# Kernel optimization log

Measured on AMD Instinct MI355X. Metric: run time of the kernel, lower is better.

Reference implementation:

```python
import jax, jax.numpy as jnp
import numpy as np

H = 128  # hidden size
I = 5    # input size


def setup_inputs() -> dict:
    key = jax.random.key(0)
    ks = jax.random.split(key, 8)
    B, T = 2048, 512
    s_ih = 1.0 / np.sqrt(H)
    x = jax.random.normal(ks[0], (B, T, I), dtype=jnp.float32)
    # PyTorch LSTM params, gate order (i, f, g, o)
    W_ih = jax.random.uniform(ks[1], (4 * H, I), jnp.float32, -s_ih, s_ih)
    W_hh = jax.random.uniform(ks[2], (4 * H, H), jnp.float32, -s_ih, s_ih)
    b_ih = jax.random.uniform(ks[3], (4 * H,), jnp.float32, -s_ih, s_ih)
    b_hh = jax.random.uniform(ks[4], (4 * H,), jnp.float32, -s_ih, s_ih)
    W_lin = jax.random.uniform(ks[5], (1, H), jnp.float32, -s_ih, s_ih)
    b_lin = jax.random.uniform(ks[6], (1,), jnp.float32, -s_ih, s_ih)
    return {"x": x, "W_ih": W_ih, "W_hh": W_hh, "b_ih": b_ih,
            "b_hh": b_hh, "W_lin": W_lin, "b_lin": b_lin}


def _lstm_final_h(x, W_ih, W_hh, b_ih, b_hh):
    B = x.shape[0]
    # Precompute input projection for all timesteps: [B, T, 4H]
    x_proj = jnp.einsum('bti,gi->btg', x, W_ih) + b_ih + b_hh

    def step(carry, xt):
        h, c = carry
        gates = xt + h @ W_hh.T  # [B, 4H]
        i, f, g, o = jnp.split(gates, 4, axis=-1)
        i = jax.nn.sigmoid(i)
        f = jax.nn.sigmoid(f)
        g = jnp.tanh(g)
        o = jax.nn.sigmoid(o)
        c = f * c + i * g
        h = o * jnp.tanh(c)
        return (h, c), None

    h0 = jnp.zeros((B, H), dtype=x.dtype)
    c0 = jnp.zeros((B, H), dtype=x.dtype)
    (h_n, _), _ = jax.lax.scan(step, (h0, c0), jnp.swapaxes(x_proj, 0, 1))
    return h_n  # [B, H]


def reference(x, W_ih, W_hh, b_ih, b_hh, W_lin, b_lin):
    h_n = _lstm_final_h(x, W_ih, W_hh, b_ih, b_hh)
    # h_n.reshape(num_layers*B, H) @ linear -> [B, 1]
    return h_n @ W_lin.T + b_lin
```

## Files before the change

### kernel.cpp

```cpp
#include <hip/hip_runtime.h>


#define HH 128
#define II 5
#define TT 512
#define BT 8
#define NT 512
#define KS 136
#define XT (TT * 8 + 8)
#define HB (16 * KS)

typedef __attribute__((ext_vector_type(8))) _Float16 half8;
typedef __attribute__((ext_vector_type(4))) _Float16 half4;
typedef __attribute__((ext_vector_type(4))) float f32x4;

#define SIG(u) __builtin_amdgcn_rcpf(1.0f + __builtin_amdgcn_exp2f(u))
#define MF32(A, B, C) __builtin_amdgcn_mfma_f32_16x16x32_f16((A), (B), (C), 0, 0, 0)
#define MF16(A, B, C) __builtin_amdgcn_mfma_f32_16x16x16f16((A), (B), (C), 0, 0, 0)
#define SGB(m, n) __builtin_amdgcn_sched_group_barrier((m), (n), 0)

#define STEP(PB, LAST) {                                                        \
    const _Float16* hp = hrd + (PB) * HB;                                       \
    ah0 = *reinterpret_cast<const half8*>(hp);                                  \
    ah1 = *reinterpret_cast<const half8*>(hp + 32);                             \
    ah2 = *reinterpret_cast<const half8*>(hp + 64);                             \
    ah3 = *reinterpret_cast<const half8*>(hp + 96);                             \
                    \
    f32x4 a0 = MF16(ax4, wfx[0], zero4);                                        \
    f32x4 a1 = MF16(ax4, wfx[1], zero4);                                        \
    f32x4 a2 = MF16(ax4, wfx[2], zero4);                                        \
    f32x4 a3 = MF16(ax4, wfx[3], zero4);                                        \
                                                     \
    a0 = MF32(ah0, wf[0][0], a0); a1 = MF32(ah0, wf[1][0], a1);                 \
    a0 = MF32(ah1, wf[0][1], a0); a1 = MF32(ah1, wf[1][1], a1);                 \
    a0 = MF32(ah2, wf[0][2], a0); a1 = MF32(ah2, wf[1][2], a1);                 \
    a0 = MF32(ah3, wf[0][3], a0); a1 = MF32(ah3, wf[1][3], a1);                 \
                  \
    float iv0 = SIG(a0[0]);                                                     \
    float iv1 = SIG(a0[1]);                                                     \
    float fv0 = SIG(a1[0]);                                                     \
    float fv1 = SIG(a1[1]);                                                     \
                                                     \
    a2 = MF32(ah0, wf[2][0], a2); a3 = MF32(ah0, wf[3][0], a3);                 \
    a2 = MF32(ah1, wf[2][1], a2); a3 = MF32(ah1, wf[3][1], a3);                 \
    a2 = MF32(ah2, wf[2][2], a2); a3 = MF32(ah2, wf[3][2], a3);                 \
    a2 = MF32(ah3, wf[2][3], a2); a3 = MF32(ah3, wf[3][3], a3);                 \
    if (!(LAST)) {                             \
        xcur += xinc;                                                           \
        ax4 = *reinterpret_cast<const half4*>(xcur);                            \
    }                                                                           \
    float gv0 = 1.0f - 2.0f * SIG(a2[0]);                                       \
    float ov0 = SIG(a3[0]);                                                     \
    cc0 = fv0 * cc0 + iv0 * gv0;                                                \
    float hv0 = ov0 * (1.0f - 2.0f * SIG(2.88539008f * cc0));                   \
    float gv1 = 1.0f - 2.0f * SIG(a2[1]);                                       \
    float ov1 = SIG(a3[1]);                                                     \
    cc1 = fv1 * cc1 + iv1 * gv1;                                                \
    float hv1 = ov1 * (1.0f - 2.0f * SIG(2.88539008f * cc1));                   \
    if (LAST) {                                                                 \
        hsc[bcell][hcol] = hv0; hsc[bcell + 1][hcol] = hv1;                     \
    } else {                                                                    \
        _Float16* wp = hwr + ((PB) ^ 1) * HB;                                   \
        wp[0]  = (_Float16)hv0;                                                 \
        wp[KS] = (_Float16)hv1;                                                 \
    }                                                                           \
     \
    SGB(0x100, 4);                                    \
    SGB(0x008, 4);               \
    SGB(0x008, 8);                                         \
    SGB(0x402, 14);                     \
    SGB(0x008, 8);                                         \
    __syncthreads();                                                            \
}

__global__ __launch_bounds__(NT)
__attribute__((amdgpu_waves_per_eu(2, 2)))
void lstm_r15(const float* __restrict__ x,
              const float* __restrict__ W_ih,
              const float* __restrict__ W_hh,
              const float* __restrict__ b_ih,
              const float* __restrict__ b_hh,
              const float* __restrict__ W_lin,
              const float* __restrict__ b_lin,
              float* __restrict__ out,
              int B)
{
    __shared__ __align__(16) _Float16 hbuf[2][16][KS];
    __shared__ __align__(16) _Float16 zrow[KS];
    __shared__ __align__(16) _Float16 xs[BT * XT];
    __shared__ float hsc[BT][HH + 4];

    const int tid  = threadIdx.x;
    const int b0   = blockIdx.x * BT;
    const int lane = tid & 63;
    const int w    = tid >> 6;
    const int n    = lane & 15;
    const int q    = lane >> 4;
    const int q8   = q * 8;
    const int hcol = w * 16 + n;

    half8 wf[4][4];
    half4 wfx[4];
    #pragma unroll
    for (int g = 0; g < 4; ++g) {
        const float sc = (g == 2) ? 2.88539008f : -1.44269504f;
        const int j = g * HH + hcol;
        #pragma unroll
        for (int kc = 0; kc < 4; ++kc) {
            const float* p = W_hh + (size_t)j * HH + kc * 32 + q8;
            #pragma unroll
            for (int e = 0; e < 8; ++e) wf[g][kc][e] = (_Float16)(p[e] * sc);
        }
        #pragma unroll
        for (int e = 0; e < 4; ++e) {
            const int k = q * 4 + e;
            float v = 0.0f;
            if (k < II)       v = W_ih[j * II + k];
            else if (k == II) v = b_ih[j] + b_hh[j];
            wfx[g][e] = (_Float16)(v * sc);
        }
    }

    for (int idx = tid; idx < 2 * 16 * KS; idx += NT)
        (&hbuf[0][0][0])[idx] = (_Float16)0.0f;
    if (tid < KS) zrow[tid] = (_Float16)0.0f;
    for (int idx = tid; idx < BT * XT; idx += NT)
        xs[idx] = (_Float16)0.0f;
    __syncthreads();

    {
        const int lb = tid & 63, bb = tid >> 6;
        if (b0 + bb < B) {
            const float* xb = x + (size_t)(b0 + bb) * TT * II;
            for (int e = lb * 4; e < TT * II; e += 256) {
                float4 v = *reinterpret_cast<const float4*>(xb + e);
                float vv[4] = {v.x, v.y, v.z, v.w};
                #pragma unroll
                for (int u = 0; u < 4; ++u) {
                    const int ee = e + u;
                    xs[bb * XT + (ee / 5) * 8 + (ee % 5)] = (_Float16)vv[u];
                }
            }
        }
        for (int s = tid; s < BT * TT; s += NT)
            xs[(s >> 9) * XT + (s & 511) * 8 + 5] = (_Float16)1.0f;
    }
    __syncthreads();

    const int bcell = 2 * q;
    float cc0 = 0.f, cc1 = 0.f;
    const f32x4 zero4 = {0.f, 0.f, 0.f, 0.f};
    const bool xreal = ((n & 2) == 0);
    const int  bofn  = (n >> 2) * 2 + (n & 1);
    const _Float16* hrd  = &hbuf[0][n][0] + q8;
    _Float16*       hwr  = &hbuf[0][q * 4][0] + hcol;
    const _Float16* xcur = xreal ? (&xs[bofn * XT] + q * 4) : (&zrow[0] + q * 4);
    const int       xinc = xreal ? 8 : 0;

    half8 ah0, ah1, ah2, ah3;
    half4 ax4 = *reinterpret_cast<const half4*>(xcur);

    #pragma unroll 1
    for (int k = 0; k < (TT - 2) / 2; ++k) {
        STEP(0, false);
        STEP(1, false);
    }
    STEP(0, false);
    STEP(1, true);

    float p = hsc[w][lane] * W_lin[lane] + hsc[w][lane + 64] * W_lin[lane + 64];
    #pragma unroll
    for (int off = 32; off > 0; off >>= 1) p += __shfl_down(p, off, 64);
    if (lane == 0 && (b0 + w) < B) out[b0 + w] = p + b_lin[0];
}

extern "C" void kernel_launch(void* const* d_in, const int* in_sizes, int n_in,
                              void* d_out, int out_size, void* d_ws, size_t ws_size,
                              hipStream_t stream) {
    const float* x     = (const float*)d_in[0];
    const float* W_ih  = (const float*)d_in[1];
    const float* W_hh  = (const float*)d_in[2];
    const float* b_ih  = (const float*)d_in[3];
    const float* b_hh  = (const float*)d_in[4];
    const float* W_lin = (const float*)d_in[5];
    const float* b_lin = (const float*)d_in[6];
    float* out = (float*)d_out;

    const int B = in_sizes[0] / (TT * II);
    const int grid = (B + BT - 1) / BT;
    lstm_r15<<<grid, NT, 0, stream>>>(x, W_ih, W_hh, b_ih, b_hh,
                                      W_lin, b_lin, out, B);
}
```

Baseline: 355.7 us.

## Halve block to four waves, each computing two hidden column tiles

Cuts the block from 8 to 4 waves. Each wave now owns 32 hidden columns (two 16-column tiles) and holds twice the W_hh fragments in registers, with waves_per_eu set to 1 to allow the larger register budget. The aim is to shrink per-step barrier cost and LDS h reads relative to MFMA work, and give each wave more independent MFMA chains to interleave with the gate math. The trade-off is doubled per-wave serial work on the recurrent critical path and lower occupancy.

```diff
diff --git a/kernel.cpp b/kernel.cpp
--- a/kernel.cpp
+++ b/kernel.cpp
@@ -5,7 +5,7 @@
 #define II 5
 #define TT 512
 #define BT 8
-#define NT 512
+#define NT 256
 #define KS 136
 #define XT (TT * 8 + 8)
 #define HB (16 * KS)
@@ -25,57 +25,92 @@
     ah1 = *reinterpret_cast<const half8*>(hp + 32);                             \
     ah2 = *reinterpret_cast<const half8*>(hp + 64);                             \
     ah3 = *reinterpret_cast<const half8*>(hp + 96);                             \
-                    \
-    f32x4 a0 = MF16(ax4, wfx[0], zero4);                                        \
-    f32x4 a1 = MF16(ax4, wfx[1], zero4);                                        \
-    f32x4 a2 = MF16(ax4, wfx[2], zero4);                                        \
-    f32x4 a3 = MF16(ax4, wfx[3], zero4);                                        \
-                                                     \
-    a0 = MF32(ah0, wf[0][0], a0); a1 = MF32(ah0, wf[1][0], a1);                 \
-    a0 = MF32(ah1, wf[0][1], a0); a1 = MF32(ah1, wf[1][1], a1);                 \
-    a0 = MF32(ah2, wf[0][2], a0); a1 = MF32(ah2, wf[1][2], a1);                 \
-    a0 = MF32(ah3, wf[0][3], a0); a1 = MF32(ah3, wf[1][3], a1);                 \
-                  \
-    float iv0 = SIG(a0[0]);                                                     \
-    float iv1 = SIG(a0[1]);                                                     \
-    float fv0 = SIG(a1[0]);                                                     \
-    float fv1 = SIG(a1[1]);                                                     \
-                                                     \
-    a2 = MF32(ah0, wf[2][0], a2); a3 = MF32(ah0, wf[3][0], a3);                 \
-    a2 = MF32(ah1, wf[2][1], a2); a3 = MF32(ah1, wf[3][1], a3);                 \
-    a2 = MF32(ah2, wf[2][2], a2); a3 = MF32(ah2, wf[3][2], a3);                 \
-    a2 = MF32(ah3, wf[2][3], a2); a3 = MF32(ah3, wf[3][3], a3);                 \
+                                   \
+    f32x4 a00 = MF16(ax4, wfx[0][0], zero4);                                    \
+    f32x4 a01 = MF16(ax4, wfx[0][1], zero4);                                    \
+    f32x4 a10 = MF16(ax4, wfx[1][0], zero4);                                    \
+    f32x4 a11 = MF16(ax4, wfx[1][1], zero4);                                    \
+    f32x4 a02 = MF16(ax4, wfx[0][2], zero4);                                    \
+    f32x4 a03 = MF16(ax4, wfx[0][3], zero4);                                    \
+    f32x4 a12 = MF16(ax4, wfx[1][2], zero4);                                    \
+    f32x4 a13 = MF16(ax4, wfx[1][3], zero4);                                    \
+                                                \
+    a00 = MF32(ah0, wf[0][0][0], a00); a01 = MF32(ah0, wf[0][1][0], a01);       \
+    a10 = MF32(ah0, wf[1][0][0], a10); a11 = MF32(ah0, wf[1][1][0], a11);       \
+    a00 = MF32(ah1, wf[0][0][1], a00); a01 = MF32(ah1, wf[0][1][1], a01);       \
+    a10 = MF32(ah1, wf[1][0][1], a10); a11 = MF32(ah1, wf[1][1][1], a11);       \
+    a00 = MF32(ah2, wf[0][0][2], a00); a01 = MF32(ah2, wf[0][1][2], a01);       \
+    a10 = MF32(ah2, wf[1][0][2], a10); a11 = MF32(ah2, wf[1][1][2], a11);       \
+    a00 = MF32(ah3, wf[0][0][3], a00); a01 = MF32(ah3, wf[0][1][3], a01);       \
+    a10 = MF32(ah3, wf[1][0][3], a10); a11 = MF32(ah3, wf[1][1][3], a11);       \
+         \
+    float iv0 = SIG(a00[0]);                                                    \
+    float iv1 = SIG(a00[1]);                                                    \
+    float fv0 = SIG(a01[0]);                                                    \
+    float fv1 = SIG(a01[1]);                                                    \
+    float iv2 = SIG(a10[0]);                                                    \
+    float iv3 = SIG(a10[1]);                                                    \
+    float fv2 = SIG(a11[0]);                                                    \
+    float fv3 = SIG(a11[1]);                                                    \
+             \
+    a02 = MF32(ah0, wf[0][2][0], a02); a03 = MF32(ah0, wf[0][3][0], a03);       \
+    a02 = MF32(ah1, wf[0][2][1], a02); a03 = MF32(ah1, wf[0][3][1], a03);       \
+    a02 = MF32(ah2, wf[0][2][2], a02); a03 = MF32(ah2, wf[0][3][2], a03);       \
+    a02 = MF32(ah3, wf[0][2][3], a02); a03 = MF32(ah3, wf[0][3][3], a03);       \
+    a12 = MF32(ah0, wf[1][2][0], a12); a13 = MF32(ah0, wf[1][3][0], a13);       \
+    a12 = MF32(ah1, wf[1][2][1], a12); a13 = MF32(ah1, wf[1][3][1], a13);       \
+    a12 = MF32(ah2, wf[1][2][2], a12); a13 = MF32(ah2, wf[1][3][2], a13);       \
+    a12 = MF32(ah3, wf[1][2][3], a12); a13 = MF32(ah3, wf[1][3][3], a13);       \
     if (!(LAST)) {                             \
         xcur += xinc;                                                           \
         ax4 = *reinterpret_cast<const half4*>(xcur);                            \
     }                                                                           \
-    float gv0 = 1.0f - 2.0f * SIG(a2[0]);                                       \
-    float ov0 = SIG(a3[0]);                                                     \
+        \
+    float gv0 = 1.0f - 2.0f * SIG(a02[0]);                                      \
+    float ov0 = SIG(a03[0]);                                                    \
     cc0 = fv0 * cc0 + iv0 * gv0;                                                \
     float hv0 = ov0 * (1.0f - 2.0f * SIG(2.88539008f * cc0));                   \
-    float gv1 = 1.0f - 2.0f * SIG(a2[1]);                                       \
-    float ov1 = SIG(a3[1]);                                                     \
+    float gv1 = 1.0f - 2.0f * SIG(a02[1]);                                      \
+    float ov1 = SIG(a03[1]);                                                    \
     cc1 = fv1 * cc1 + iv1 * gv1;                                                \
     float hv1 = ov1 * (1.0f - 2.0f * SIG(2.88539008f * cc1));                   \
+    float gv2 = 1.0f - 2.0f * SIG(a12[0]);                                      \
+    float ov2 = SIG(a13[0]);                                                    \
+    cc2 = fv2 * cc2 + iv2 * gv2;                                                \
+    float hv2 = ov2 * (1.0f - 2.0f * SIG(2.88539008f * cc2));                   \
+    float gv3 = 1.0f - 2.0f * SIG(a12[1]);                                      \
+    float ov3 = SIG(a13[1]);                                                    \
+    cc3 = fv3 * cc3 + iv3 * gv3;                                                \
+    float hv3 = ov3 * (1.0f - 2.0f * SIG(2.88539008f * cc3));                   \
     if (LAST) {                                                                 \
-        hsc[bcell][hcol] = hv0; hsc[bcell + 1][hcol] = hv1;                     \
+        hsc[bcell][hcol0] = hv0; hsc[bcell + 1][hcol0] = hv1;                   \
+        hsc[bcell][hcol1] = hv2; hsc[bcell + 1][hcol1] = hv3;                   \
     } else {                                                                    \
-        _Float16* wp = hwr + ((PB) ^ 1) * HB;                                   \
-        wp[0]  = (_Float16)hv0;                                                 \
-        wp[KS] = (_Float16)hv1;                                                 \
+        _Float16* wp0 = hwr0 + ((PB) ^ 1) * HB;                                 \
+        _Float16* wp1 = hwr1 + ((PB) ^ 1) * HB;                                 \
+        wp0[0]  = (_Float16)hv0;                                                \
+        wp0[KS] = (_Float16)hv1;                                                \
+        wp1[0]  = (_Float16)hv2;                                                \
+        wp1[KS] = (_Float16)hv3;                                                \
     }                                                                           \
-     \
+      \
     SGB(0x100, 4);                                    \
-    SGB(0x008, 4);               \
-    SGB(0x008, 8);                                         \
-    SGB(0x402, 14);                     \
-    SGB(0x008, 8);                                         \
+    SGB(0x008, 8);                                \
+    SGB(0x008, 16);                                   \
+    SGB(0x008, 2); SGB(0x402, 6);                \
+    SGB(0x008, 2); SGB(0x402, 6);              \
+    SGB(0x008, 2); SGB(0x402, 6);              \
+    SGB(0x008, 2); SGB(0x402, 6);                    \
+    SGB(0x008, 2); SGB(0x402, 6);                                               \
+    SGB(0x008, 2); SGB(0x402, 6);                                               \
+    SGB(0x008, 2); SGB(0x402, 6);                                               \
+    SGB(0x008, 2); SGB(0x402, 6);                                               \
     __syncthreads();                                                            \
 }
 
 __global__ __launch_bounds__(NT)
-__attribute__((amdgpu_waves_per_eu(2, 2)))
-void lstm_r15(const float* __restrict__ x,
+__attribute__((amdgpu_waves_per_eu(1, 1)))
+void lstm_r16(const float* __restrict__ x,
               const float* __restrict__ W_ih,
               const float* __restrict__ W_hh,
               const float* __restrict__ b_ih,
@@ -97,42 +132,47 @@
     const int n    = lane & 15;
     const int q    = lane >> 4;
     const int q8   = q * 8;
-    const int hcol = w * 16 + n;
-
-    half8 wf[4][4];
-    half4 wfx[4];
+    const int hcol0 = w * 32 + n;
+    const int hcol1 = w * 32 + 16 + n;
+
+    half8 wf[2][4][4];
+    half4 wfx[2][4];
     #pragma unroll
-    for (int g = 0; g < 4; ++g) {
-        const float sc = (g == 2) ? 2.88539008f : -1.44269504f;
-        const int j = g * HH + hcol;
+    for (int c = 0; c < 2; ++c) {
+        const int hc = w * 32 + c * 16 + n;
         #pragma unroll
-        for (int kc = 0; kc < 4; ++kc) {
-            const float* p = W_hh + (size_t)j * HH + kc * 32 + q8;
+        for (int g = 0; g < 4; ++g) {
+            const float sc = (g == 2) ? 2.88539008f : -1.44269504f;
+            const int j = g * HH + hc;
             #pragma unroll
-            for (int e = 0; e < 8; ++e) wf[g][kc][e] = (_Float16)(p[e] * sc);
-        }
-        #pragma unroll
-        for (int e = 0; e < 4; ++e) {
-            const int k = q * 4 + e;
-            float v = 0.0f;
-            if (k < II)       v = W_ih[j * II + k];
-            else if (k == II) v = b_ih[j] + b_hh[j];
-            wfx[g][e] = (_Float16)(v * sc);
+            for (int kc = 0; kc < 4; ++kc) {
+                const float* p = W_hh + (size_t)j * HH + kc * 32 + q8;
+                #pragma unroll
+                for (int e = 0; e < 8; ++e) wf[c][g][kc][e] = (_Float16)(p[e] * sc);
+            }
+            #pragma unroll
+            for (int e = 0; e < 4; ++e) {
+                const int k = q * 4 + e;
+                float v = 0.0f;
+                if (k < II)       v = W_ih[j * II + k];
+                else if (k == II) v = b_ih[j] + b_hh[j];
+                wfx[c][g][e] = (_Float16)(v * sc);
+            }
         }
     }
 
     for (int idx = tid; idx < 2 * 16 * KS; idx += NT)
         (&hbuf[0][0][0])[idx] = (_Float16)0.0f;
-    if (tid < KS) zrow[tid] = (_Float16)0.0f;
+    for (int idx = tid; idx < KS; idx += NT) zrow[idx] = (_Float16)0.0f;
     for (int idx = tid; idx < BT * XT; idx += NT)
         xs[idx] = (_Float16)0.0f;
     __syncthreads();
 
     {
-        const int lb = tid & 63, bb = tid >> 6;
+        const int lb = tid & 31, bb = tid >> 5;
         if (b0 + bb < B) {
             const float* xb = x + (size_t)(b0 + bb) * TT * II;
-            for (int e = lb * 4; e < TT * II; e += 256) {
+            for (int e = lb * 4; e < TT * II; e += 128) {
                 float4 v = *reinterpret_cast<const float4*>(xb + e);
                 float vv[4] = {v.x, v.y, v.z, v.w};
                 #pragma unroll
@@ -148,12 +188,13 @@
     __syncthreads();
 
     const int bcell = 2 * q;
-    float cc0 = 0.f, cc1 = 0.f;
+    float cc0 = 0.f, cc1 = 0.f, cc2 = 0.f, cc3 = 0.f;
     const f32x4 zero4 = {0.f, 0.f, 0.f, 0.f};
     const bool xreal = ((n & 2) == 0);
     const int  bofn  = (n >> 2) * 2 + (n & 1);
     const _Float16* hrd  = &hbuf[0][n][0] + q8;
-    _Float16*       hwr  = &hbuf[0][q * 4][0] + hcol;
+    _Float16*       hwr0 = &hbuf[0][q * 4][0] + hcol0;
+    _Float16*       hwr1 = &hbuf[0][q * 4][0] + hcol1;
     const _Float16* xcur = xreal ? (&xs[bofn * XT] + q * 4) : (&zrow[0] + q * 4);
     const int       xinc = xreal ? 8 : 0;
 
@@ -168,10 +209,14 @@
     STEP(0, false);
     STEP(1, true);
 
-    float p = hsc[w][lane] * W_lin[lane] + hsc[w][lane + 64] * W_lin[lane + 64];
     #pragma unroll
-    for (int off = 32; off > 0; off >>= 1) p += __shfl_down(p, off, 64);
-    if (lane == 0 && (b0 + w) < B) out[b0 + w] = p + b_lin[0];
+    for (int rep = 0; rep < 2; ++rep) {
+        const int bb = w * 2 + rep;
+        float p = hsc[bb][lane] * W_lin[lane] + hsc[bb][lane + 64] * W_lin[lane + 64];
+        #pragma unroll
+        for (int off = 32; off > 0; off >>= 1) p += __shfl_down(p, off, 64);
+        if (lane == 0 && (b0 + bb) < B) out[b0 + bb] = p + b_lin[0];
+    }
 }
 
 extern "C" void kernel_launch(void* const* d_in, const int* in_sizes, int n_in,
@@ -188,6 +233,6 @@
 
     const int B = in_sizes[0] / (TT * II);
     const int grid = (B + BT - 1) / BT;
-    lstm_r15<<<grid, NT, 0, stream>>>(x, W_ih, W_hh, b_ih, b_hh,
+    lstm_r16<<<grid, NT, 0, stream>>>(x, W_ih, W_hh, b_ih, b_hh,
                                       W_lin, b_lin, out, B);
 }
```

After: 405.4 us. 14.0% more time.
